# Performance work log

Measured on AMD Instinct MI355X. Metric: run time of the kernel, lower is better.

Reference implementation:

```python
import jax, jax.numpy as jnp
import numpy as np

NUM_EMBEDDINGS = 1024
EMBEDDING_DIM = 64
COMMITMENT_COST = 0.25
EPS_NORM = 1e-12  # torch F.normalize eps


def _l2_normalize(x):
    n = jnp.linalg.norm(x, axis=-1, keepdims=True)
    return x / jnp.maximum(n, EPS_NORM)


def setup_inputs() -> dict:
    key = jax.random.key(0)
    k1, k2 = jax.random.split(key)
    inputs = jax.random.normal(k1, (16, 4096, EMBEDDING_DIM), dtype=jnp.float32)
    weight = jax.random.normal(k2, (NUM_EMBEDDINGS, EMBEDDING_DIM), dtype=jnp.float32) * 0.02
    return {"inputs": inputs, "weight": weight}


def reference(inputs, weight):
    input_shape = inputs.shape
    x = _l2_normalize(inputs)                      # [B,S,D]
    flat = x.reshape(-1, EMBEDDING_DIM)            # [N,D]
    w = _l2_normalize(weight)                      # [K,D]

    distances = (jnp.sum(flat ** 2, axis=1, keepdims=True)
                 + jnp.sum(w ** 2, axis=1)
                 - 2.0 * flat @ w.T)               # [N,K]
    encoding_indices = jnp.argmin(distances, axis=1)  # [N]

    quantized = w[encoding_indices].reshape(input_shape)  # [B,S,D]

    e_latent_loss = jnp.mean((jax.lax.stop_gradient(quantized) - x) ** 2)
    q_latent_loss = jnp.mean((quantized - jax.lax.stop_gradient(x)) ** 2)
    loss = q_latent_loss + COMMITMENT_COST * e_latent_loss

    # straight-through estimator
    quantized_ste = x + jax.lax.stop_gradient(quantized - x)

    # perplexity (no-grad bookkeeping)
    n = encoding_indices.shape[0]
    counts = jnp.zeros((NUM_EMBEDDINGS,), jnp.float32).at[encoding_indices].add(1.0)
    avg_probs = counts / n
    perplexity = jnp.exp(-jnp.sum(avg_probs * jnp.log(avg_probs + 1e-10)))

    return loss, quantized_ste, perplexity, encoding_indices[:, None]
```

## Files before the change

kernel.cpp:

```cpp
#include <hip/hip_runtime.h>
#include <hip/hip_bf16.h>
#include <math.h>

#define NROWS   65536
#define DIM     64
#define KCODES  1024
#define RPB     64
#define NBLOCKS (NROWS / RPB)

#define QGAP 1.25e-4f

typedef short short8 __attribute__((ext_vector_type(8)));
typedef float f32x4  __attribute__((ext_vector_type(4)));

#define OUT_Q_OFF    ((size_t)1)
#define OUT_PERP_OFF ((size_t)(1 + (size_t)NROWS * DIM))
#define OUT_IDX_OFF  ((size_t)(2 + (size_t)NROWS * DIM))

#define WS_COUNTS 0
#define WS_SSEC   4096
#define WS_DONE   4100
#define WS_WN     8192
#define WS_SK     (WS_WN + KCODES*DIM*4)
#define WS_WNH    (WS_SK + KCODES*4)
#define WS_WNL    (WS_WNH + KCODES*DIM*2)

__device__ __forceinline__ unsigned short bf16_rne(float f) {
  unsigned u = __float_as_uint(f);
  return (unsigned short)((u + 0x7FFFu + ((u >> 16) & 1u)) >> 16);
}
__device__ __forceinline__ float bf16f(unsigned short h) {
  return __uint_as_float(((unsigned)h) << 16);
}

__global__ void __launch_bounds__(64) normalize_w_kernel(
    const float* __restrict__ w, float* __restrict__ wn, float* __restrict__ sk,
    unsigned short* __restrict__ wnh, unsigned short* __restrict__ wnl,
    unsigned* __restrict__ counts, float* __restrict__ sse_accum,
    unsigned* __restrict__ done) {
  const int k = blockIdx.x;
  const int d = threadIdx.x;
  if (d == 0) {
    counts[k] = 0u;
    if (k == 0) { *sse_accum = 0.f; *done = 0u; }
  }
  float v = w[k * DIM + d];
  float ss = v * v;
  #pragma unroll
  for (int o = 32; o > 0; o >>= 1) ss += __shfl_xor(ss, o, 64);
  const float den = fmaxf(sqrtf(ss), 1e-12f);
  const float q = v / den;
  wn[k * DIM + d] = q;
  const unsigned short h = bf16_rne(q);
  wnh[k * DIM + d] = h;
  wnl[k * DIM + d] = bf16_rne(q - bf16f(h));
  float s2 = q * q;
  #pragma unroll
  for (int o = 32; o > 0; o >>= 1) s2 += __shfl_xor(s2, o, 64);
  if (d == 0) sk[k] = s2;
}

__global__ void __launch_bounds__(256) vq_mega_kernel(
    const float* __restrict__ x, const unsigned short* __restrict__ wnh,
    const unsigned short* __restrict__ wnl, const float* __restrict__ sk,
    const float* __restrict__ wn, float* __restrict__ out,
    unsigned* __restrict__ counts, float* __restrict__ sse_accum,
    unsigned* __restrict__ done) {
  __shared__ unsigned AB[9216];
  __shared__ float skb[2][64];
  __shared__ float c_arr[RPB];
  __shared__ float rowsse[RPB];
  __shared__ int   ib[RPB];
  __shared__ int   qlist[RPB];
  __shared__ int   flist[RPB];
  __shared__ int   qn_s, fn_s;
  __shared__ int   islast;
  const int tid = threadIdx.x;
  const int lane = tid & 63, wave = tid >> 6;

  if (tid == 0) { qn_s = 0; fn_s = 0; }

  {
    const int row_l = tid >> 2;
    const int qr = tid & 3;
    const size_t row = (size_t)blockIdx.x * RPB + row_l;
    const float4* xr = (const float4*)(x + row * DIM) + qr * 4;
    float4 xv[4];
    float ss = 0.f;
    #pragma unroll
    for (int i = 0; i < 4; i++) {
      xv[i] = xr[i];
      ss += xv[i].x * xv[i].x + xv[i].y * xv[i].y + xv[i].z * xv[i].z + xv[i].w * xv[i].w;
    }
    ss += __shfl_xor(ss, 1, 64); ss += __shfl_xor(ss, 2, 64);
    const float inv = 1.0f / fmaxf(sqrtf(ss), 1e-12f);
    float c = 0.f;
    #pragma unroll
    for (int i = 0; i < 4; i++) {
      const float a0 = xv[i].x * inv, a1 = xv[i].y * inv;
      const float a2 = xv[i].z * inv, a3 = xv[i].w * inv;
      c += a0 * a0 + a1 * a1 + a2 * a2 + a3 * a3;
      const unsigned short h0 = bf16_rne(a0), h1 = bf16_rne(a1);
      const unsigned short h2 = bf16_rne(a2), h3 = bf16_rne(a3);
      const unsigned short l0 = bf16_rne(a0 - bf16f(h0)), l1 = bf16_rne(a1 - bf16f(h1));
      const unsigned short l2 = bf16_rne(a2 - bf16f(h2)), l3 = bf16_rne(a3 - bf16f(h3));
      AB[row_l * 36 + qr * 8 + 2 * i]            = (unsigned)h0 | ((unsigned)h1 << 16);
      AB[row_l * 36 + qr * 8 + 2 * i + 1]        = (unsigned)h2 | ((unsigned)h3 << 16);
      AB[2304 + row_l * 36 + qr * 8 + 2 * i]     = (unsigned)l0 | ((unsigned)l1 << 16);
      AB[2304 + row_l * 36 + qr * 8 + 2 * i + 1] = (unsigned)l2 | ((unsigned)l3 << 16);
    }
    c += __shfl_xor(c, 1, 64); c += __shfl_xor(c, 2, 64);
    if (qr == 0) c_arr[row_l] = c;
  }
  __syncthreads();

  short8 ah[2], al[2];
  #pragma unroll
  for (int kk = 0; kk < 2; kk++) {
    const int r = wave * 16 + (lane & 15);
    ah[kk] = *(const short8*)&AB[r * 36 + kk * 16 + (lane >> 4) * 4];
    al[kk] = *(const short8*)&AB[2304 + r * 36 + kk * 16 + (lane >> 4) * 4];
  }
  __syncthreads();

  float d1[4], d2[4], d3[4];
  int   i1[4], i2[4];
  #pragma unroll
  for (int s = 0; s < 4; s++) {
    d1[s] = INFINITY; d2[s] = INFINITY; d3[s] = INFINITY;
    i1[s] = 0x7FFFFFFF; i2[s] = 0x7FFFFFFF;
  }

  {
    const int code = tid >> 2, q = tid & 3;
    const float4* gh = (const float4*)(wnh + (size_t)code * DIM + q * 16);
    const float4* gl = (const float4*)(wnl + (size_t)code * DIM + q * 16);
    float4* dh = (float4*)&AB[code * 36 + q * 8];
    float4* dl = (float4*)&AB[2304 + code * 36 + q * 8];
    dh[0] = gh[0]; dh[1] = gh[1];
    dl[0] = gl[0]; dl[1] = gl[1];
    if (tid < 64) skb[0][tid] = sk[tid];
  }

  #pragma unroll 2
  for (int c = 0; c < 16; c++) {
    const int b = c & 1;
    __syncthreads();
    if (c < 15) {
      const int nb = b ^ 1;
      const int code = tid >> 2, q = tid & 3;
      const float4* gh = (const float4*)(wnh + (size_t)((c + 1) * 64 + code) * DIM + q * 16);
      const float4* gl = (const float4*)(wnl + (size_t)((c + 1) * 64 + code) * DIM + q * 16);
      float4* dh = (float4*)&AB[nb * 4608 + code * 36 + q * 8];
      float4* dl = (float4*)&AB[nb * 4608 + 2304 + code * 36 + q * 8];
      dh[0] = gh[0]; dh[1] = gh[1];
      dl[0] = gl[0]; dl[1] = gl[1];
      if (tid < 64) skb[nb][tid] = sk[(c + 1) * 64 + tid];
    }
    #pragma unroll
    for (int tt = 0; tt < 4; tt++) {
      const int cb = tt * 16 + (lane & 15);
      const float skv = skb[b][cb];
      const int codev = c * 64 + cb;
      const short8 bh0 = *(const short8*)&AB[b * 4608 + cb * 36 + 0 * 16 + (lane >> 4) * 4];
      const short8 bh1 = *(const short8*)&AB[b * 4608 + cb * 36 + 1 * 16 + (lane >> 4) * 4];
      const short8 bl0 = *(const short8*)&AB[b * 4608 + 2304 + cb * 36 + 0 * 16 + (lane >> 4) * 4];
      const short8 bl1 = *(const short8*)&AB[b * 4608 + 2304 + cb * 36 + 1 * 16 + (lane >> 4) * 4];
      f32x4 acc = {0.f, 0.f, 0.f, 0.f};
      acc = __builtin_amdgcn_mfma_f32_16x16x32_bf16(ah[0], bh0, acc, 0, 0, 0);
      acc = __builtin_amdgcn_mfma_f32_16x16x32_bf16(ah[1], bh1, acc, 0, 0, 0);
      acc = __builtin_amdgcn_mfma_f32_16x16x32_bf16(al[0], bh0, acc, 0, 0, 0);
      acc = __builtin_amdgcn_mfma_f32_16x16x32_bf16(al[1], bh1, acc, 0, 0, 0);
      acc = __builtin_amdgcn_mfma_f32_16x16x32_bf16(ah[0], bl0, acc, 0, 0, 0);
      acc = __builtin_amdgcn_mfma_f32_16x16x32_bf16(ah[1], bl1, acc, 0, 0, 0);
      #pragma unroll
      for (int i = 0; i < 4; i++) {
        const float dist = fmaf(-2.0f, acc[i], skv);
        const int s = i;
        d3[s] = __builtin_amdgcn_fmed3f(d2[s], d3[s], fmaxf(d1[s], dist));
        const bool lt2 = dist < d2[s];
        i2[s] = lt2 ? codev : i2[s];
        d2[s] = __builtin_amdgcn_fmed3f(d1[s], d2[s], dist);
        const bool lt1 = dist < d1[s];
        i2[s] = lt1 ? i1[s] : i2[s];
        i1[s] = lt1 ? codev : i1[s];
        d1[s] = lt1 ? dist : d1[s];
      }
    }
  }

  #pragma unroll
  for (int s = 0; s < 4; s++) {
    float a1 = d1[s], a2 = d2[s], a3 = d3[s];
    int   ai = i1[s], ai2 = i2[s];
    #pragma unroll
    for (int m = 1; m < 16; m <<= 1) {
      const float p1 = __shfl_xor(a1, m, 64);
      const float p2 = __shfl_xor(a2, m, 64);
      const float p3 = __shfl_xor(a3, m, 64);
      const int   pi = __shfl_xor(ai, m, 64);
      const int   pi2 = __shfl_xor(ai2, m, 64);
      const bool take = (p1 < a1) || (p1 == a1 && pi < ai);
      const float lo1 = take ? p1 : a1, lo2 = take ? p2 : a2, lo3 = take ? p3 : a3;
      const float hi1 = take ? a1 : p1, hi2 = take ? a2 : p2;
      const int   loi = take ? pi : ai, loi2 = take ? pi2 : ai2;
      const int   hii = take ? ai : pi;
      const bool c2 = hi1 < lo2;
      a1 = lo1; ai = loi;
      a2 = c2 ? hi1 : lo2; ai2 = c2 ? hii : loi2;
      a3 = c2 ? fminf(lo2, hi2) : fminf(lo3, hi1);
    }
    if ((lane & 15) == 0) {
      const int row_local = wave * 16 + (lane >> 4) * 4 + s;
      ib[row_local] = ai;
      rowsse[row_local] = a1 + c_arr[row_local];
      if (a3 - a1 < QGAP) {
        flist[atomicAdd(&fn_s, 1)] = row_local;
      } else if (a2 - a1 < QGAP) {
        qlist[atomicAdd(&qn_s, 1)] = row_local | (ai << 6) | (ai2 << 16);
      }
    }
  }
  __syncthreads();

  const int qn = qn_s, fn = fn_s;
  if (tid < qn) {
    const int packed = qlist[tid];
    const int rl = packed & 63;
    const int c1 = (packed >> 6) & 1023, c2i = (packed >> 16) & 1023;
    const size_t row = (size_t)blockIdx.x * RPB + rl;
    const float4* xr = (const float4*)(x + row * DIM);
    float4 xv[16];
    float ss = 0.f;
    #pragma unroll
    for (int i = 0; i < 16; i++) {
      xv[i] = xr[i];
      ss += xv[i].x * xv[i].x + xv[i].y * xv[i].y + xv[i].z * xv[i].z + xv[i].w * xv[i].w;
    }
    const float den = fmaxf(sqrtf(ss), 1e-12f);
    #pragma unroll
    for (int i = 0; i < 16; i++) { xv[i].x /= den; xv[i].y /= den; xv[i].z /= den; xv[i].w /= den; }
    float cc = 0.f;
    #pragma unroll
    for (int i = 0; i < 16; i++)
      cc += xv[i].x * xv[i].x + xv[i].y * xv[i].y + xv[i].z * xv[i].z + xv[i].w * xv[i].w;
    float dd[2]; const int cand[2] = {c1, c2i};
    #pragma unroll
    for (int t = 0; t < 2; t++) {
      const float4* wr = (const float4*)(wn + (size_t)cand[t] * DIM);
      float e0 = 0.f, e1 = 0.f, e2 = 0.f, e3 = 0.f;
      #pragma unroll
      for (int i = 0; i < 16; i++) {
        const float4 wv = wr[i];
        e0 = fmaf(xv[i].x, wv.x, e0);
        e1 = fmaf(xv[i].y, wv.y, e1);
        e2 = fmaf(xv[i].z, wv.z, e2);
        e3 = fmaf(xv[i].w, wv.w, e3);
      }
      dd[t] = (cc + sk[cand[t]]) - 2.0f * ((e0 + e1) + (e2 + e3));
    }
    const bool tb = (dd[1] < dd[0]) || (dd[1] == dd[0] && c2i < c1);
    ib[rl] = tb ? c2i : c1;
    rowsse[rl] = tb ? dd[1] : dd[0];
  }

  for (int qi = wave; qi < fn; qi += 4) {
    const int rl = flist[qi];
    const size_t row = (size_t)blockIdx.x * RPB + rl;
    const float4* xr = (const float4*)(x + row * DIM);
    float4 xv[16];
    float ss = 0.f;
    #pragma unroll
    for (int i = 0; i < 16; i++) {
      xv[i] = xr[i];
      ss += xv[i].x * xv[i].x + xv[i].y * xv[i].y + xv[i].z * xv[i].z + xv[i].w * xv[i].w;
    }
    const float den = fmaxf(sqrtf(ss), 1e-12f);
    #pragma unroll
    for (int i = 0; i < 16; i++) { xv[i].x /= den; xv[i].y /= den; xv[i].z /= den; xv[i].w /= den; }
    float cc = 0.f;
    #pragma unroll
    for (int i = 0; i < 16; i++)
      cc += xv[i].x * xv[i].x + xv[i].y * xv[i].y + xv[i].z * xv[i].z + xv[i].w * xv[i].w;

    float best = INFINITY;
    int bidx = 0x7FFFFFFF;
    for (int j = 0; j < 16; j++) {
      const int k = j * 64 + lane;
      const float4* wr = (const float4*)(wn + (size_t)k * DIM);
      float e0 = 0.f, e1 = 0.f, e2 = 0.f, e3 = 0.f;
      #pragma unroll
      for (int i = 0; i < 16; i++) {
        const float4 wv = wr[i];
        e0 = fmaf(xv[i].x, wv.x, e0);
        e1 = fmaf(xv[i].y, wv.y, e1);
        e2 = fmaf(xv[i].z, wv.z, e2);
        e3 = fmaf(xv[i].w, wv.w, e3);
      }
      const float dot = (e0 + e1) + (e2 + e3);
      const float dist = (cc + sk[k]) - 2.0f * dot;
      if (dist < best) { best = dist; bidx = k; }
    }
    #pragma unroll
    for (int m = 1; m < 64; m <<= 1) {
      const float pb = __shfl_xor(best, m, 64);
      const int pi = __shfl_xor(bidx, m, 64);
      if (pb < best || (pb == best && pi < bidx)) { best = pb; bidx = pi; }
    }
    if (lane == 0) { ib[rl] = bidx; rowsse[rl] = best; }
  }
  __syncthreads();

  if (tid < RPB) {
    const size_t row = (size_t)blockIdx.x * RPB + tid;
    const int idx = ib[tid];
    out[OUT_IDX_OFF + row] = (float)idx;
    atomicAdd(&counts[idx], 1u);
  }

  const size_t obase = OUT_Q_OFF + (size_t)blockIdx.x * (RPB * DIM);
  #pragma unroll 4
  for (int j = 0; j < 16; j++) {
    const int e = j * 256 + tid;
    out[obase + e] = wn[(size_t)ib[e >> 6] * DIM + (e & 63)];
  }

  __syncthreads();
  for (int s = 32; s > 0; s >>= 1) {
    if (tid < s) rowsse[tid] += rowsse[tid + s];
    __syncthreads();
  }
  if (tid == 0) atomicAdd(sse_accum, rowsse[0]);

  if (tid == 0) {
    __threadfence();
    islast = (atomicAdd(done, 1u) == NBLOCKS - 1) ? 1 : 0;
  }
  __syncthreads();
  if (islast) {
    __threadfence();
    float h = 0.f;
    #pragma unroll
    for (int i = 0; i < 4; i++) {
      const float cv = (float)counts[tid * 4 + i];
      const float avg = cv * (1.0f / (float)NROWS);
      h += avg * logf(avg + 1e-10f);
    }
    #pragma unroll
    for (int o = 32; o > 0; o >>= 1) h += __shfl_xor(h, o, 64);
    __shared__ float hred[4];
    if (lane == 0) hred[wave] = h;
    __syncthreads();
    if (tid == 0) {
      const float H = -(hred[0] + hred[1] + hred[2] + hred[3]);
      const float mse = *sse_accum * (1.0f / (float)((size_t)NROWS * DIM));
      out[0] = mse + 0.25f * mse;
      out[OUT_PERP_OFF] = expf(H);
    }
  }
}

extern "C" void kernel_launch(void* const* d_in, const int* in_sizes, int n_in,
                              void* d_out, int out_size, void* d_ws, size_t ws_size,
                              hipStream_t stream) {
  const float* x = (const float*)d_in[0];
  const float* w = (const float*)d_in[1];
  float* out = (float*)d_out;

  char* ws = (char*)d_ws;
  unsigned* counts    = (unsigned*)(ws + WS_COUNTS);
  float* sse_accum    = (float*)(ws + WS_SSEC);
  unsigned* done      = (unsigned*)(ws + WS_DONE);
  float* wn           = (float*)(ws + WS_WN);
  float* sk           = (float*)(ws + WS_SK);
  unsigned short* wnh = (unsigned short*)(ws + WS_WNH);
  unsigned short* wnl = (unsigned short*)(ws + WS_WNL);

  normalize_w_kernel<<<KCODES, 64, 0, stream>>>(w, wn, sk, wnh, wnl,
                                                counts, sse_accum, done);
  vq_mega_kernel<<<NBLOCKS, 256, 0, stream>>>(
      x, wnh, wnl, sk, wn, out, counts, sse_accum, done);
}
```

Baseline: 157.0 us.

## Process 128 rows per block and track argmin with packed integer keys

```diff
diff --git a/kernel.cpp b/kernel.cpp
--- a/kernel.cpp
+++ b/kernel.cpp
@@ -5,10 +5,10 @@
 #define NROWS   65536
 #define DIM     64
 #define KCODES  1024
-#define RPB     64
+#define RPB     128
 #define NBLOCKS (NROWS / RPB)
 
-#define QGAP 1.25e-4f
+#define NEXACT 9u
 
 typedef short short8 __attribute__((ext_vector_type(8)));
 typedef float f32x4  __attribute__((ext_vector_type(4)));
@@ -31,6 +31,11 @@
 }
 __device__ __forceinline__ float bf16f(unsigned short h) {
   return __uint_as_float(((unsigned)h) << 16);
+}
+__device__ __forceinline__ unsigned med3u(unsigned a, unsigned b, unsigned c) {
+  unsigned d;
+  asm("v_med3_u32 %0, %1, %2, %3" : "=v"(d) : "v"(a), "v"(b), "v"(c));
+  return d;
 }
 
 __global__ void __launch_bounds__(64) normalize_w_kernel(
@@ -81,22 +86,22 @@
   if (tid == 0) { qn_s = 0; fn_s = 0; }
 
   {
-    const int row_l = tid >> 2;
-    const int qr = tid & 3;
+    const int row_l = tid >> 1;
+    const int half = tid & 1;
     const size_t row = (size_t)blockIdx.x * RPB + row_l;
-    const float4* xr = (const float4*)(x + row * DIM) + qr * 4;
-    float4 xv[4];
+    const float4* xr = (const float4*)(x + row * DIM) + half * 8;
+    float4 xv[8];
     float ss = 0.f;
     #pragma unroll
-    for (int i = 0; i < 4; i++) {
+    for (int i = 0; i < 8; i++) {
       xv[i] = xr[i];
       ss += xv[i].x * xv[i].x + xv[i].y * xv[i].y + xv[i].z * xv[i].z + xv[i].w * xv[i].w;
     }
-    ss += __shfl_xor(ss, 1, 64); ss += __shfl_xor(ss, 2, 64);
+    ss += __shfl_xor(ss, 1, 64);
     const float inv = 1.0f / fmaxf(sqrtf(ss), 1e-12f);
     float c = 0.f;
     #pragma unroll
-    for (int i = 0; i < 4; i++) {
+    for (int i = 0; i < 8; i++) {
       const float a0 = xv[i].x * inv, a1 = xv[i].y * inv;
       const float a2 = xv[i].z * inv, a3 = xv[i].w * inv;
       c += a0 * a0 + a1 * a1 + a2 * a2 + a3 * a3;
@@ -104,32 +109,30 @@
       const unsigned short h2 = bf16_rne(a2), h3 = bf16_rne(a3);
       const unsigned short l0 = bf16_rne(a0 - bf16f(h0)), l1 = bf16_rne(a1 - bf16f(h1));
       const unsigned short l2 = bf16_rne(a2 - bf16f(h2)), l3 = bf16_rne(a3 - bf16f(h3));
-      AB[row_l * 36 + qr * 8 + 2 * i]            = (unsigned)h0 | ((unsigned)h1 << 16);
-      AB[row_l * 36 + qr * 8 + 2 * i + 1]        = (unsigned)h2 | ((unsigned)h3 << 16);
-      AB[2304 + row_l * 36 + qr * 8 + 2 * i]     = (unsigned)l0 | ((unsigned)l1 << 16);
-      AB[2304 + row_l * 36 + qr * 8 + 2 * i + 1] = (unsigned)l2 | ((unsigned)l3 << 16);
-    }
-    c += __shfl_xor(c, 1, 64); c += __shfl_xor(c, 2, 64);
-    if (qr == 0) c_arr[row_l] = c;
-  }
-  __syncthreads();
-
-  short8 ah[2], al[2];
-  #pragma unroll
-  for (int kk = 0; kk < 2; kk++) {
-    const int r = wave * 16 + (lane & 15);
-    ah[kk] = *(const short8*)&AB[r * 36 + kk * 16 + (lane >> 4) * 4];
-    al[kk] = *(const short8*)&AB[2304 + r * 36 + kk * 16 + (lane >> 4) * 4];
-  }
-  __syncthreads();
-
-  float d1[4], d2[4], d3[4];
-  int   i1[4], i2[4];
-  #pragma unroll
-  for (int s = 0; s < 4; s++) {
-    d1[s] = INFINITY; d2[s] = INFINITY; d3[s] = INFINITY;
-    i1[s] = 0x7FFFFFFF; i2[s] = 0x7FFFFFFF;
-  }
+      AB[row_l * 36 + half * 16 + 2 * i]            = (unsigned)h0 | ((unsigned)h1 << 16);
+      AB[row_l * 36 + half * 16 + 2 * i + 1]        = (unsigned)h2 | ((unsigned)h3 << 16);
+      AB[4608 + row_l * 36 + half * 16 + 2 * i]     = (unsigned)l0 | ((unsigned)l1 << 16);
+      AB[4608 + row_l * 36 + half * 16 + 2 * i + 1] = (unsigned)l2 | ((unsigned)l3 << 16);
+    }
+    c += __shfl_xor(c, 1, 64);
+    if (half == 0) c_arr[row_l] = c;
+  }
+  __syncthreads();
+
+  short8 ah[2][2], al[2][2];
+  #pragma unroll
+  for (int rt = 0; rt < 2; rt++)
+    #pragma unroll
+    for (int kk = 0; kk < 2; kk++) {
+      const int r = wave * 32 + rt * 16 + (lane & 15);
+      ah[rt][kk] = *(const short8*)&AB[r * 36 + kk * 16 + (lane >> 4) * 4];
+      al[rt][kk] = *(const short8*)&AB[4608 + r * 36 + kk * 16 + (lane >> 4) * 4];
+    }
+  __syncthreads();
+
+  unsigned k1[8], k2[8], k3[8];
+  #pragma unroll
+  for (int s = 0; s < 8; s++) { k1[s] = 0xFFFFFFFFu; k2[s] = 0xFFFFFFFFu; k3[s] = 0xFFFFFFFFu; }
 
   {
     const int code = tid >> 2, q = tid & 3;
@@ -139,7 +142,7 @@
     float4* dl = (float4*)&AB[2304 + code * 36 + q * 8];
     dh[0] = gh[0]; dh[1] = gh[1];
     dl[0] = gl[0]; dl[1] = gl[1];
-    if (tid < 64) skb[0][tid] = sk[tid];
+    if (tid < 64) skb[0][tid] = sk[tid] + 4.0f;
   }
 
   #pragma unroll 2
@@ -155,69 +158,71 @@
       float4* dl = (float4*)&AB[nb * 4608 + 2304 + code * 36 + q * 8];
       dh[0] = gh[0]; dh[1] = gh[1];
       dl[0] = gl[0]; dl[1] = gl[1];
-      if (tid < 64) skb[nb][tid] = sk[(c + 1) * 64 + tid];
+      if (tid < 64) skb[nb][tid] = sk[(c + 1) * 64 + tid] + 4.0f;
     }
     #pragma unroll
     for (int tt = 0; tt < 4; tt++) {
       const int cb = tt * 16 + (lane & 15);
-      const float skv = skb[b][cb];
-      const int codev = c * 64 + cb;
+      const float skv4 = skb[b][cb];
+      const unsigned chi = (unsigned)(c * 4 + tt);
       const short8 bh0 = *(const short8*)&AB[b * 4608 + cb * 36 + 0 * 16 + (lane >> 4) * 4];
       const short8 bh1 = *(const short8*)&AB[b * 4608 + cb * 36 + 1 * 16 + (lane >> 4) * 4];
       const short8 bl0 = *(const short8*)&AB[b * 4608 + 2304 + cb * 36 + 0 * 16 + (lane >> 4) * 4];
       const short8 bl1 = *(const short8*)&AB[b * 4608 + 2304 + cb * 36 + 1 * 16 + (lane >> 4) * 4];
-      f32x4 acc = {0.f, 0.f, 0.f, 0.f};
-      acc = __builtin_amdgcn_mfma_f32_16x16x32_bf16(ah[0], bh0, acc, 0, 0, 0);
-      acc = __builtin_amdgcn_mfma_f32_16x16x32_bf16(ah[1], bh1, acc, 0, 0, 0);
-      acc = __builtin_amdgcn_mfma_f32_16x16x32_bf16(al[0], bh0, acc, 0, 0, 0);
-      acc = __builtin_amdgcn_mfma_f32_16x16x32_bf16(al[1], bh1, acc, 0, 0, 0);
-      acc = __builtin_amdgcn_mfma_f32_16x16x32_bf16(ah[0], bl0, acc, 0, 0, 0);
-      acc = __builtin_amdgcn_mfma_f32_16x16x32_bf16(ah[1], bl1, acc, 0, 0, 0);
       #pragma unroll
-      for (int i = 0; i < 4; i++) {
-        const float dist = fmaf(-2.0f, acc[i], skv);
-        const int s = i;
-        d3[s] = __builtin_amdgcn_fmed3f(d2[s], d3[s], fmaxf(d1[s], dist));
-        const bool lt2 = dist < d2[s];
-        i2[s] = lt2 ? codev : i2[s];
-        d2[s] = __builtin_amdgcn_fmed3f(d1[s], d2[s], dist);
-        const bool lt1 = dist < d1[s];
-        i2[s] = lt1 ? i1[s] : i2[s];
-        i1[s] = lt1 ? codev : i1[s];
-        d1[s] = lt1 ? dist : d1[s];
+      for (int rt = 0; rt < 2; rt++) {
+        f32x4 acc = {0.f, 0.f, 0.f, 0.f};
+        acc = __builtin_amdgcn_mfma_f32_16x16x32_bf16(ah[rt][0], bh0, acc, 0, 0, 0);
+        acc = __builtin_amdgcn_mfma_f32_16x16x32_bf16(ah[rt][1], bh1, acc, 0, 0, 0);
+        acc = __builtin_amdgcn_mfma_f32_16x16x32_bf16(al[rt][0], bh0, acc, 0, 0, 0);
+        acc = __builtin_amdgcn_mfma_f32_16x16x32_bf16(al[rt][1], bh1, acc, 0, 0, 0);
+        acc = __builtin_amdgcn_mfma_f32_16x16x32_bf16(ah[rt][0], bl0, acc, 0, 0, 0);
+        acc = __builtin_amdgcn_mfma_f32_16x16x32_bf16(ah[rt][1], bl1, acc, 0, 0, 0);
+        #pragma unroll
+        for (int i = 0; i < 4; i++) {
+          const float dist4 = fmaf(-2.0f, acc[i], skv4);
+          const unsigned key = (__float_as_uint(dist4) & 0xFFFFFFC0u) | chi;
+          const int s = rt * 4 + i;
+          const unsigned t = (k1[s] > key) ? k1[s] : key;
+          k3[s] = med3u(k2[s], k3[s], t);
+          k2[s] = med3u(k1[s], k2[s], key);
+          k1[s] = (key < k1[s]) ? key : k1[s];
+        }
       }
     }
   }
 
   #pragma unroll
-  for (int s = 0; s < 4; s++) {
-    float a1 = d1[s], a2 = d2[s], a3 = d3[s];
-    int   ai = i1[s], ai2 = i2[s];
+  for (int s = 0; s < 8; s++) {
+    unsigned a1 = (k1[s] << 4) | (unsigned)(lane & 15);
+    unsigned a2 = (k2[s] << 4) | (unsigned)(lane & 15);
+    unsigned a3 = (k3[s] << 4) | (unsigned)(lane & 15);
     #pragma unroll
     for (int m = 1; m < 16; m <<= 1) {
-      const float p1 = __shfl_xor(a1, m, 64);
-      const float p2 = __shfl_xor(a2, m, 64);
-      const float p3 = __shfl_xor(a3, m, 64);
-      const int   pi = __shfl_xor(ai, m, 64);
-      const int   pi2 = __shfl_xor(ai2, m, 64);
-      const bool take = (p1 < a1) || (p1 == a1 && pi < ai);
-      const float lo1 = take ? p1 : a1, lo2 = take ? p2 : a2, lo3 = take ? p3 : a3;
-      const float hi1 = take ? a1 : p1, hi2 = take ? a2 : p2;
-      const int   loi = take ? pi : ai, loi2 = take ? pi2 : ai2;
-      const int   hii = take ? ai : pi;
-      const bool c2 = hi1 < lo2;
-      a1 = lo1; ai = loi;
-      a2 = c2 ? hi1 : lo2; ai2 = c2 ? hii : loi2;
-      a3 = c2 ? fminf(lo2, hi2) : fminf(lo3, hi1);
+      const unsigned p1 = (unsigned)__shfl_xor((int)a1, m, 64);
+      const unsigned p2 = (unsigned)__shfl_xor((int)a2, m, 64);
+      const unsigned p3 = (unsigned)__shfl_xor((int)a3, m, 64);
+      const unsigned th = (a1 > p1) ? a1 : p1;
+      const unsigned n1 = (a1 < p1) ? a1 : p1;
+      const unsigned m2 = (a2 < p2) ? a2 : p2;
+      const unsigned m3 = (a3 < p3) ? a3 : p3;
+      const unsigned hi = (th > m2) ? th : m2;
+      a1 = n1;
+      a2 = (th < m2) ? th : m2;
+      const unsigned md = med3u(th, m2, m3);
+      a3 = (hi < md) ? hi : md;
     }
     if ((lane & 15) == 0) {
-      const int row_local = wave * 16 + (lane >> 4) * 4 + s;
-      ib[row_local] = ai;
-      rowsse[row_local] = a1 + c_arr[row_local];
-      if (a3 - a1 < QGAP) {
+      const int row_local = wave * 32 + (s >> 2) * 16 + (lane >> 4) * 4 + (s & 3);
+      const int i1 = (int)(a1 & 1023u);
+      ib[row_local] = i1;
+      const unsigned ub = ((a1 & 0xFFFFFC00u) >> 4) | 0x40000000u;
+      rowsse[row_local] = __uint_as_float(ub) - 4.0f + c_arr[row_local] + 1.6e-5f;
+      const unsigned b1 = a1 >> 10, b2 = a2 >> 10, b3 = a3 >> 10;
+      if (b3 - b1 < NEXACT) {
         flist[atomicAdd(&fn_s, 1)] = row_local;
-      } else if (a2 - a1 < QGAP) {
-        qlist[atomicAdd(&qn_s, 1)] = row_local | (ai << 6) | (ai2 << 16);
+      } else if (b2 - b1 < NEXACT) {
+        qlist[atomicAdd(&qn_s, 1)] = row_local | (i1 << 7) | ((int)(a2 & 1023u) << 17);
       }
     }
   }
@@ -226,8 +231,8 @@
   const int qn = qn_s, fn = fn_s;
   if (tid < qn) {
     const int packed = qlist[tid];
-    const int rl = packed & 63;
-    const int c1 = (packed >> 6) & 1023, c2i = (packed >> 16) & 1023;
+    const int rl = packed & 127;
+    const int c1 = (packed >> 7) & 1023, c2i = (packed >> 17) & 1023;
     const size_t row = (size_t)blockIdx.x * RPB + rl;
     const float4* xr = (const float4*)(x + row * DIM);
     float4 xv[16];
@@ -320,13 +325,13 @@
 
   const size_t obase = OUT_Q_OFF + (size_t)blockIdx.x * (RPB * DIM);
   #pragma unroll 4
-  for (int j = 0; j < 16; j++) {
+  for (int j = 0; j < 32; j++) {
     const int e = j * 256 + tid;
     out[obase + e] = wn[(size_t)ib[e >> 6] * DIM + (e & 63)];
   }
 
   __syncthreads();
-  for (int s = 32; s > 0; s >>= 1) {
+  for (int s = 64; s > 0; s >>= 1) {
     if (tid < s) rowsse[tid] += rowsse[tid + s];
     __syncthreads();
   }
```

Measured after the change: 130.0 us. 1.21x faster.
